# Optimization experiments

Measured on AMD Instinct MI355X. Metric: run time of the kernel, lower is better.

The kernel has to match this reference:

```python
import jax, jax.numpy as jnp
import numpy as np

NUM_CLASSES = 20
NUM_ANCHORS = 5
INPUT_SIZE = 320.0
CONF_THR = 0.5
IOU_THR = 0.5
EPS = 1e-6
H = W = 40


def setup_inputs() -> dict:
    key = jax.random.key(0)
    x = jax.random.normal(key, (1, NUM_ANCHORS * (5 + NUM_CLASSES), H, W), dtype=jnp.float32)
    scaled_anchors = jnp.array(
        [[1.3221, 1.73145], [3.19275, 4.00944], [5.05587, 8.09892],
         [9.47112, 4.84053], [11.2364, 10.0071]], dtype=jnp.float32)
    return {"x": x, "scaled_anchors": scaled_anchors}


def decode(x, anchors):
    # x: (B, A*(5+C), H, W) -> boxes (B, A*H*W, 6) = [cx, cy, w, h, conf, cls]
    B, _, h, w = x.shape
    A = anchors.shape[0]
    stride_h = INPUT_SIZE / h
    stride_w = INPUT_SIZE / w
    pred = x.reshape(B, A, 5 + NUM_CLASSES, h, w).transpose(0, 1, 3, 4, 2)  # (B,A,H,W,5+C)
    tx = jax.nn.sigmoid(pred[..., 0])
    ty = jax.nn.sigmoid(pred[..., 1])
    tw = pred[..., 2]
    th = pred[..., 3]
    conf = jax.nn.sigmoid(pred[..., 4])
    cls_idx = jnp.argmax(jax.nn.sigmoid(pred[..., 5:]), axis=-1)  # (B,A,H,W)
    grid_x = jnp.arange(w, dtype=x.dtype)            # broadcasts along last axis
    grid_y = jnp.arange(h, dtype=x.dtype)[:, None]   # broadcasts along row axis
    aw = anchors[:, 0][None, :, None, None]
    ah = anchors[:, 1][None, :, None, None]
    bx = (tx + grid_x) * stride_w
    by = (ty + grid_y) * stride_h
    bw = jnp.exp(tw) * aw * stride_w
    bh = jnp.exp(th) * ah * stride_h
    boxes = jnp.stack([bx, by, bw, bh, conf], axis=-1).reshape(B, -1, 5)
    cls_f = cls_idx.reshape(B, -1, 1).astype(x.dtype)
    return jnp.concatenate([boxes, cls_f], axis=-1)


def nms(boxes6):
    # boxes6: (N, 6) [cx, cy, w, h, conf, cls]. Fixed-shape NMS: boxes are
    # sorted by conf desc; suppressed / low-conf boxes are zeroed out.
    order = jnp.argsort(-boxes6[:, 4])
    b = boxes6[order]
    valid = b[:, 4] > CONF_THR
    cx, cy, w, h, cls = b[:, 0], b[:, 1], b[:, 2], b[:, 3], b[:, 5]
    x1, y1 = cx - w / 2.0, cy - h / 2.0
    x2, y2 = cx + w / 2.0, cy + h / 2.0
    inter_w = jnp.clip(jnp.minimum(x2[:, None], x2[None, :]) - jnp.maximum(x1[:, None], x1[None, :]), 0)
    inter_h = jnp.clip(jnp.minimum(y2[:, None], y2[None, :]) - jnp.maximum(y1[:, None], y1[None, :]), 0)
    inter = inter_w * inter_h                       # (N, N)
    area = jnp.abs((x2 - x1) * (y2 - y1))
    iou = inter / (area[:, None] + area[None, :] - inter + EPS)
    N = b.shape[0]
    idx = jnp.arange(N)

    def body(i, keep):
        # kept box i suppresses later boxes of the same class with IoU >= thr
        sup = keep[i] & keep & (cls == cls[i]) & (iou[i] >= IOU_THR) & (idx > i)
        return keep & ~sup

    keep = jax.lax.fori_loop(0, N, body, valid)
    return b * keep[:, None].astype(b.dtype)


def reference(x, scaled_anchors):
    dec = decode(x, scaled_anchors)   # (1, N, 6)
    return nms(dec[0])                # (N, 6)
```

## Files before the change

### kernel.cpp

```cpp
#include <hip/hip_runtime.h>
#include <stdint.h>

#define NBOX 8000
#define NPAD 8192

#define ECNT_OFF 0
#define SB(i)    (0x10000 + (size_t)(i) * 0x8000)
#define EDGE_OFF (size_t)0x200000

__device__ __forceinline__ float sigmoidf_(float x) {
    return 1.0f / (1.0f + expf(-x));
}

__global__ __launch_bounds__(512) void sort_decode_kernel(const float* __restrict__ x,
                                                          const float* __restrict__ anchors,
                                                          unsigned char* __restrict__ ws) {
    __shared__ unsigned long long keys[NPAD];
    __shared__ int partial[512];
    int tid  = threadIdx.x;
    int lane = tid & 63;
    int wv   = tid >> 6;
    int b    = blockIdx.x;

    if (b == 0 && tid == 0) *(unsigned int*)(ws + ECNT_OFF) = 0u;

    for (int t = tid; t < NPAD; t += 512) {
        unsigned long long k;
        if (t < NBOX) {
            int a = t / 1600, pos = t - a * 1600;
            float c = sigmoidf_(x[a * 40000 + 4 * 1600 + pos]);
            k = ((unsigned long long)__float_as_uint(c) << 32) | (unsigned long long)(8191 - t);
        } else {
            k = (unsigned long long)(8191 - t);
        }
        keys[t] = k;
    }
    __syncthreads();

    int i = (b << 6) + lane;
    unsigned long long ki = keys[i];
    const unsigned long long* ks = &keys[wv << 10];
    int cnt = 0;
    #pragma unroll 8
    for (int jj = 0; jj < 1024; ++jj) cnt += (ks[jj] > ki) ? 1 : 0;
    partial[(wv << 6) + lane] = cnt;
    __syncthreads();

    if (wv == 0) {
        int r = 0;
        #pragma unroll
        for (int s = 0; s < 8; ++s) r += partial[(s << 6) + lane];

        float bx = 0.f, by = 0.f, bw = 0.f, bh = 0.f, conf = 0.f, cls = -1.0f;
        if (i < NBOX) {
            int a = i / 1600, pos = i - a * 1600;
            int gy = pos / 40, gx = pos - gy * 40;
            const float* p = x + (size_t)a * 40000 + pos;
            float tx = sigmoidf_(p[0]);
            float ty = sigmoidf_(p[1600]);
            float tw = p[2 * 1600];
            float th = p[3 * 1600];
            conf = sigmoidf_(p[4 * 1600]);
            float best = -1.0f; int bi = 0;
            #pragma unroll
            for (int c = 0; c < 20; ++c) {
                float v = sigmoidf_(p[(5 + c) * 1600]);
                if (v > best) { best = v; bi = c; }
            }
            float aw = anchors[a * 2 + 0];
            float ah = anchors[a * 2 + 1];
            bx = (tx + (float)gx) * 8.0f;
            by = (ty + (float)gy) * 8.0f;
            bw = expf(tw) * aw * 8.0f;
            bh = expf(th) * ah * 8.0f;
            cls = (float)bi;
        }
        {
        #pragma clang fp contract(off)
            float x1 = bx - bw / 2.0f, y1 = by - bh / 2.0f;
            float x2 = bx + bw / 2.0f, y2 = by + bh / 2.0f;
            float ar = fabsf((x2 - x1) * (y2 - y1));
            ((float*)(ws + SB(0)))[r]  = bx;  ((float*)(ws + SB(1)))[r]  = by;
            ((float*)(ws + SB(2)))[r]  = bw;  ((float*)(ws + SB(3)))[r]  = bh;
            ((float*)(ws + SB(4)))[r]  = conf; ((float*)(ws + SB(5)))[r] = cls;
            ((float*)(ws + SB(6)))[r]  = x1;  ((float*)(ws + SB(7)))[r]  = y1;
            ((float*)(ws + SB(8)))[r]  = x2;  ((float*)(ws + SB(9)))[r]  = y2;
            ((float*)(ws + SB(10)))[r] = ar;
        }
    }
}

__global__ __launch_bounds__(256) void mask_kernel(unsigned char* __restrict__ ws) {
#pragma clang fp contract(off)
    const float* sconf = (const float*)(ws + SB(4));
    int i0 = blockIdx.y * 256;
    int w  = blockIdx.x;
    int j0 = w * 64;
    if (sconf[i0] <= 0.5f) return;
    if (sconf[j0] <= 0.5f) return;
    if (j0 + 64 <= i0) return;
    int tid  = threadIdx.x;
    int lane = tid & 63;
    int i    = i0 + tid;

    const float* sx1 = (const float*)(ws + SB(6));
    const float* sy1 = (const float*)(ws + SB(7));
    const float* sx2 = (const float*)(ws + SB(8));
    const float* sy2 = (const float*)(ws + SB(9));
    const float* sar = (const float*)(ws + SB(10));
    const float* scl = (const float*)(ws + SB(5));

    __shared__ float cx1[64], cy1[64], cx2[64], cy2[64], car[64], ccl[64], ccf[64];
    if (tid < 64) {
        int j = j0 + tid;
        cx1[tid] = sx1[j]; cy1[tid] = sy1[j];
        cx2[tid] = sx2[j]; cy2[tid] = sy2[j];
        car[tid] = sar[j]; ccl[tid] = scl[j]; ccf[tid] = sconf[j];
    }
    __syncthreads();

    unsigned long long word = 0;
    if (sconf[i] > 0.5f && j0 + 64 > i + 1) {
        float x1i = sx1[i], y1i = sy1[i], x2i = sx2[i], y2i = sy2[i];
        float ai = sar[i], ci = scl[i];
        for (int jj = 0; jj < 64; ++jj) {
            int j = j0 + jj;
            if (j <= i) continue;
            if (ccf[jj] <= 0.5f) continue;
            if (ccl[jj] != ci) continue;
            float iw = fminf(x2i, cx2[jj]) - fmaxf(x1i, cx1[jj]);
            iw = fmaxf(iw, 0.0f);
            float ih = fminf(y2i, cy2[jj]) - fmaxf(y1i, cy1[jj]);
            ih = fmaxf(ih, 0.0f);
            float inter = iw * ih;
            float denom = ai + car[jj] - inter + 1e-6f;
            if (inter / denom >= 0.5f) word |= (1ull << jj);
        }
    }

    int pc = __popcll(word);
    int scan = pc;
    #pragma unroll
    for (int d = 1; d < 64; d <<= 1) {
        int t = __shfl_up(scan, d, 64);
        if (lane >= d) scan += t;
    }
    int total = __shfl(scan, 63, 64);
    if (total > 0) {
        unsigned int base = 0;
        if (lane == 63)
            base = atomicAdd((unsigned int*)(ws + ECNT_OFF), (unsigned int)total);
        base = (unsigned int)__shfl((int)base, 63, 64);
        unsigned int off = base + (unsigned int)(scan - pc);
        unsigned int* edges = (unsigned int*)(ws + EDGE_OFF);
        unsigned long long t = word;
        while (t) {
            int bit = __builtin_ctzll(t);
            t &= t - 1ull;
            edges[off++] = ((unsigned int)i << 13) | (unsigned int)(j0 + bit);
        }
    }
}

__global__ __launch_bounds__(1024, 1) void nms_out_kernel(unsigned char* __restrict__ ws,
                                                          float* __restrict__ out) {
    int tid  = threadIdx.x;
    int lane = tid & 63;
    unsigned int E = *(const unsigned int*)(ws + ECNT_OFF);
    const unsigned int* edges = (const unsigned int*)(ws + EDGE_OFF);
    const float* sconf = (const float*)(ws + SB(4));

    __shared__ unsigned long long valid[128], alive[128], supp[128];
    __shared__ int flag;

    for (int c = tid >> 6; c < 128; c += 16) {
        unsigned long long m = __ballot(sconf[(c << 6) + lane] > 0.5f);
        if (lane == 0) valid[c] = m;
    }
    __syncthreads();
    if (tid < 128) alive[tid] = valid[tid];
    __syncthreads();

    for (;;) {
        if (tid < 128) supp[tid] = 0ull;
        __syncthreads();
        for (unsigned int e = tid; e < E; e += 1024) {
            unsigned int u = edges[e];
            unsigned int i = u >> 13, j = u & 8191u;
            if ((alive[i >> 6] >> (i & 63)) & 1ull)
                atomicOr(&supp[j >> 6], 1ull << (j & 63));
        }
        if (tid == 0) flag = 0;
        __syncthreads();
        if (tid < 128) {
            unsigned long long na = valid[tid] & ~supp[tid];
            if (na != alive[tid]) { alive[tid] = na; flag = 1; }
        }
        __syncthreads();
        if (!flag) break;
    }

    for (int r = tid; r < NBOX; r += 1024) {
        bool keep = (alive[r >> 6] >> (r & 63)) & 1ull;
        float o0 = 0.f, o1 = 0.f, o2 = 0.f, o3 = 0.f, o4 = 0.f, o5 = 0.f;
        if (keep) {
            o0 = ((const float*)(ws + SB(0)))[r];
            o1 = ((const float*)(ws + SB(1)))[r];
            o2 = ((const float*)(ws + SB(2)))[r];
            o3 = ((const float*)(ws + SB(3)))[r];
            o4 = ((const float*)(ws + SB(4)))[r];
            o5 = ((const float*)(ws + SB(5)))[r];
        }
        out[r * 6 + 0] = o0;
        out[r * 6 + 1] = o1;
        out[r * 6 + 2] = o2;
        out[r * 6 + 3] = o3;
        out[r * 6 + 4] = o4;
        out[r * 6 + 5] = o5;
    }
}

extern "C" void kernel_launch(void* const* d_in, const int* in_sizes, int n_in,
                              void* d_out, int out_size, void* d_ws, size_t ws_size,
                              hipStream_t stream) {
    const float* x       = (const float*)d_in[0];
    const float* anchors = (const float*)d_in[1];
    float* out           = (float*)d_out;
    unsigned char* ws    = (unsigned char*)d_ws;

    sort_decode_kernel<<<NPAD / 64, 512, 0, stream>>>(x, anchors, ws);
    dim3 mgrid(128, NPAD / 256);
    mask_kernel<<<mgrid, 256, 0, stream>>>(ws);
    nms_out_kernel<<<1, 1024, 0, stream>>>(ws, out);
}
```

Measured before the change: 120.2 us.

## Fuse mask and NMS kernels via last-block-done pattern with shared edge cache

Merges the IoU edge-building kernel and the single-block iterative NMS/output kernel into one launch. The last block to finish, found through an atomic done counter, runs the suppression fixed-point loop. It first copies the edge list into LDS when the edge count fits, so each iteration reads edges from LDS instead of global memory. Mask blocks grow to 1024 threads covering 1024 rows each, which cuts the block count but gives coarser early-exit skipping and a heavier per-block LDS footprint.

```diff
diff --git a/kernel.cpp b/kernel.cpp
--- a/kernel.cpp
+++ b/kernel.cpp
@@ -3,8 +3,10 @@
 
 #define NBOX 8000
 #define NPAD 8192
+#define ECAP 16384
 
 #define ECNT_OFF 0
+#define DONE_OFF 4
 #define SB(i)    (0x10000 + (size_t)(i) * 0x8000)
 #define EDGE_OFF (size_t)0x200000
 
@@ -22,7 +24,8 @@
     int wv   = tid >> 6;
     int b    = blockIdx.x;
 
-    if (b == 0 && tid == 0) *(unsigned int*)(ws + ECNT_OFF) = 0u;
+    if (b == 0 && tid == 0)
+        *(unsigned long long*)(ws + ECNT_OFF) = 0ull;
 
     for (int t = tid; t < NPAD; t += 512) {
         unsigned long long k;
@@ -90,93 +93,103 @@
     }
 }
 
-__global__ __launch_bounds__(256) void mask_kernel(unsigned char* __restrict__ ws) {
+__global__ __launch_bounds__(1024) void mask_nms_kernel(unsigned char* __restrict__ ws,
+                                                        float* __restrict__ out) {
 #pragma clang fp contract(off)
+    __shared__ float cx1[64], cy1[64], cx2[64], cy2[64], car[64], ccl[64], ccf[64];
+    __shared__ unsigned int eshare[ECAP];
+    __shared__ unsigned long long valid[128], alive[128], supp[128];
+    __shared__ int flag, isLast;
+
     const float* sconf = (const float*)(ws + SB(4));
-    int i0 = blockIdx.y * 256;
-    int w  = blockIdx.x;
-    int j0 = w * 64;
-    if (sconf[i0] <= 0.5f) return;
-    if (sconf[j0] <= 0.5f) return;
-    if (j0 + 64 <= i0) return;
     int tid  = threadIdx.x;
     int lane = tid & 63;
-    int i    = i0 + tid;
-
-    const float* sx1 = (const float*)(ws + SB(6));
-    const float* sy1 = (const float*)(ws + SB(7));
-    const float* sx2 = (const float*)(ws + SB(8));
-    const float* sy2 = (const float*)(ws + SB(9));
-    const float* sar = (const float*)(ws + SB(10));
-    const float* scl = (const float*)(ws + SB(5));
-
-    __shared__ float cx1[64], cy1[64], cx2[64], cy2[64], car[64], ccl[64], ccf[64];
-    if (tid < 64) {
-        int j = j0 + tid;
-        cx1[tid] = sx1[j]; cy1[tid] = sy1[j];
-        cx2[tid] = sx2[j]; cy2[tid] = sy2[j];
-        car[tid] = sar[j]; ccl[tid] = scl[j]; ccf[tid] = sconf[j];
-    }
-    __syncthreads();
-
-    unsigned long long word = 0;
-    if (sconf[i] > 0.5f && j0 + 64 > i + 1) {
-        float x1i = sx1[i], y1i = sy1[i], x2i = sx2[i], y2i = sy2[i];
-        float ai = sar[i], ci = scl[i];
-        for (int jj = 0; jj < 64; ++jj) {
-            int j = j0 + jj;
-            if (j <= i) continue;
-            if (ccf[jj] <= 0.5f) continue;
-            if (ccl[jj] != ci) continue;
-            float iw = fminf(x2i, cx2[jj]) - fmaxf(x1i, cx1[jj]);
-            iw = fmaxf(iw, 0.0f);
-            float ih = fminf(y2i, cy2[jj]) - fmaxf(y1i, cy1[jj]);
-            ih = fmaxf(ih, 0.0f);
-            float inter = iw * ih;
-            float denom = ai + car[jj] - inter + 1e-6f;
-            if (inter / denom >= 0.5f) word |= (1ull << jj);
-        }
-    }
-
-    int pc = __popcll(word);
-    int scan = pc;
-    #pragma unroll
-    for (int d = 1; d < 64; d <<= 1) {
-        int t = __shfl_up(scan, d, 64);
-        if (lane >= d) scan += t;
-    }
-    int total = __shfl(scan, 63, 64);
-    if (total > 0) {
-        unsigned int base = 0;
-        if (lane == 63)
-            base = atomicAdd((unsigned int*)(ws + ECNT_OFF), (unsigned int)total);
-        base = (unsigned int)__shfl((int)base, 63, 64);
-        unsigned int off = base + (unsigned int)(scan - pc);
-        unsigned int* edges = (unsigned int*)(ws + EDGE_OFF);
-        unsigned long long t = word;
-        while (t) {
-            int bit = __builtin_ctzll(t);
-            t &= t - 1ull;
-            edges[off++] = ((unsigned int)i << 13) | (unsigned int)(j0 + bit);
-        }
-    }
-}
-
-__global__ __launch_bounds__(1024, 1) void nms_out_kernel(unsigned char* __restrict__ ws,
-                                                          float* __restrict__ out) {
-    int tid  = threadIdx.x;
-    int lane = tid & 63;
-    unsigned int E = *(const unsigned int*)(ws + ECNT_OFF);
+    int w  = blockIdx.x;
+    int it = blockIdx.y;
+    int i0 = it << 10;
+    int j0 = w << 6;
+
+    bool skip = (sconf[i0] <= 0.5f) | (sconf[j0] <= 0.5f) | (j0 + 64 <= i0);
+    if (!skip) {
+        const float* sx1 = (const float*)(ws + SB(6));
+        const float* sy1 = (const float*)(ws + SB(7));
+        const float* sx2 = (const float*)(ws + SB(8));
+        const float* sy2 = (const float*)(ws + SB(9));
+        const float* sar = (const float*)(ws + SB(10));
+        const float* scl = (const float*)(ws + SB(5));
+        if (tid < 64) {
+            int j = j0 + tid;
+            cx1[tid] = sx1[j]; cy1[tid] = sy1[j];
+            cx2[tid] = sx2[j]; cy2[tid] = sy2[j];
+            car[tid] = sar[j]; ccl[tid] = scl[j]; ccf[tid] = sconf[j];
+        }
+        __syncthreads();
+
+        int i = i0 + tid;
+        unsigned long long word = 0;
+        if (sconf[i] > 0.5f && j0 + 64 > i + 1) {
+            float x1i = sx1[i], y1i = sy1[i], x2i = sx2[i], y2i = sy2[i];
+            float ai = sar[i], ci = scl[i];
+            for (int jj = 0; jj < 64; ++jj) {
+                int j = j0 + jj;
+                if (j <= i) continue;
+                if (ccf[jj] <= 0.5f) continue;
+                if (ccl[jj] != ci) continue;
+                float iw = fminf(x2i, cx2[jj]) - fmaxf(x1i, cx1[jj]);
+                iw = fmaxf(iw, 0.0f);
+                float ih = fminf(y2i, cy2[jj]) - fmaxf(y1i, cy1[jj]);
+                ih = fmaxf(ih, 0.0f);
+                float inter = iw * ih;
+                float denom = ai + car[jj] - inter + 1e-6f;
+                if (inter / denom >= 0.5f) word |= (1ull << jj);
+            }
+        }
+
+        int pc = __popcll(word);
+        int scan = pc;
+        #pragma unroll
+        for (int d = 1; d < 64; d <<= 1) {
+            int t = __shfl_up(scan, d, 64);
+            if (lane >= d) scan += t;
+        }
+        int total = __shfl(scan, 63, 64);
+        if (total > 0) {
+            unsigned int base = 0;
+            if (lane == 63)
+                base = atomicAdd((unsigned int*)(ws + ECNT_OFF), (unsigned int)total);
+            base = (unsigned int)__shfl((int)base, 63, 64);
+            unsigned int off = base + (unsigned int)(scan - pc);
+            unsigned int* edges = (unsigned int*)(ws + EDGE_OFF);
+            unsigned long long t = word;
+            int i_ = i0 + tid;
+            while (t) {
+                int bit = __builtin_ctzll(t);
+                t &= t - 1ull;
+                edges[off++] = ((unsigned int)i_ << 13) | (unsigned int)(j0 + bit);
+            }
+        }
+    }
+
+    __syncthreads();
+    if (tid == 0) {
+        __threadfence();
+        unsigned int old = __hip_atomic_fetch_add((unsigned int*)(ws + DONE_OFF), 1u,
+                                                  __ATOMIC_ACQ_REL, __HIP_MEMORY_SCOPE_AGENT);
+        isLast = (old == (int)(128 * 8 - 1));
+    }
+    __syncthreads();
+    if (!isLast) return;
+    __threadfence();
+
+    unsigned int E = *(volatile unsigned int*)(ws + ECNT_OFF);
     const unsigned int* edges = (const unsigned int*)(ws + EDGE_OFF);
-    const float* sconf = (const float*)(ws + SB(4));
-
-    __shared__ unsigned long long valid[128], alive[128], supp[128];
-    __shared__ int flag;
 
     for (int c = tid >> 6; c < 128; c += 16) {
         unsigned long long m = __ballot(sconf[(c << 6) + lane] > 0.5f);
         if (lane == 0) valid[c] = m;
     }
+    bool inl = (E <= (unsigned int)ECAP);
+    if (inl) for (unsigned int e = tid; e < E; e += 1024) eshare[e] = edges[e];
     __syncthreads();
     if (tid < 128) alive[tid] = valid[tid];
     __syncthreads();
@@ -185,7 +198,7 @@
         if (tid < 128) supp[tid] = 0ull;
         __syncthreads();
         for (unsigned int e = tid; e < E; e += 1024) {
-            unsigned int u = edges[e];
+            unsigned int u = inl ? eshare[e] : edges[e];
             unsigned int i = u >> 13, j = u & 8191u;
             if ((alive[i >> 6] >> (i & 63)) & 1ull)
                 atomicOr(&supp[j >> 6], 1ull << (j & 63));
@@ -229,7 +242,6 @@
     unsigned char* ws    = (unsigned char*)d_ws;
 
     sort_decode_kernel<<<NPAD / 64, 512, 0, stream>>>(x, anchors, ws);
-    dim3 mgrid(128, NPAD / 256);
-    mask_kernel<<<mgrid, 256, 0, stream>>>(ws);
-    nms_out_kernel<<<1, 1024, 0, stream>>>(ws, out);
-}
+    dim3 mgrid(128, 8);
+    mask_nms_kernel<<<mgrid, 1024, 0, stream>>>(ws, out);
+}
```

New measurement: 129.8 us. +8.0%, slower.

## Resolve NMS suppression segment-by-segment with register-cached edges

Applied to the files above, without the earlier changes.

Replaces the global fixed-point iteration over all suppression edges with a segmented sweep. The 8192 sorted boxes are split into 16 segments of 512, each segment is iterated to convergence using only its internal edges, and then its surviving boxes push suppression forward to later segments. Edges are cached in per-thread registers when there are at most 16384 of them, so repeated passes avoid global reloads. This is meant to cut the number of full-edge-list passes, but every segment now scans all cached edges and pays barrier overhead, and register use rises. The old global loop is kept as a fallback for larger edge counts.

```diff
diff --git a/kernel.cpp b/kernel.cpp
--- a/kernel.cpp
+++ b/kernel.cpp
@@ -3,6 +3,9 @@
 
 #define NBOX 8000
 #define NPAD 8192
+#define ECAP 16384
+#define SEGW 8
+#define NSEG 16
 
 #define ECNT_OFF 0
 #define SB(i)    (0x10000 + (size_t)(i) * 0x8000)
@@ -167,37 +170,86 @@
     int tid  = threadIdx.x;
     int lane = tid & 63;
     unsigned int E = *(const unsigned int*)(ws + ECNT_OFF);
-    const unsigned int* edges = (const unsigned int*)(ws + EDGE_OFF);
+    const unsigned int* gedges = (const unsigned int*)(ws + EDGE_OFF);
     const float* sconf = (const float*)(ws + SB(4));
 
-    __shared__ unsigned long long valid[128], alive[128], supp[128];
+    __shared__ unsigned long long valid[128], alive[128], suppExt[128], suppInt[SEGW];
     __shared__ int flag;
 
     for (int c = tid >> 6; c < 128; c += 16) {
         unsigned long long m = __ballot(sconf[(c << 6) + lane] > 0.5f);
         if (lane == 0) valid[c] = m;
     }
+    if (tid < 128) suppExt[tid] = 0ull;
     __syncthreads();
     if (tid < 128) alive[tid] = valid[tid];
     __syncthreads();
 
-    for (;;) {
-        if (tid < 128) supp[tid] = 0ull;
-        __syncthreads();
-        for (unsigned int e = tid; e < E; e += 1024) {
-            unsigned int u = edges[e];
-            unsigned int i = u >> 13, j = u & 8191u;
-            if ((alive[i >> 6] >> (i & 63)) & 1ull)
-                atomicOr(&supp[j >> 6], 1ull << (j & 63));
-        }
-        if (tid == 0) flag = 0;
-        __syncthreads();
-        if (tid < 128) {
-            unsigned long long na = valid[tid] & ~supp[tid];
-            if (na != alive[tid]) { alive[tid] = na; flag = 1; }
-        }
-        __syncthreads();
-        if (!flag) break;
+    if (E <= (unsigned int)ECAP) {
+        unsigned int eu[ECAP / 1024];
+        int ne = 0;
+        for (unsigned int e = tid; e < E; e += 1024) eu[ne++] = gedges[e];
+
+        for (int s = 0; s < NSEG; ++s) {
+            bool segv = false;
+            #pragma unroll
+            for (int k = 0; k < SEGW; ++k) segv |= (valid[s * SEGW + k] != 0ull);
+            if (!segv) continue;
+
+            for (;;) {
+                if (tid < SEGW) suppInt[tid] = 0ull;
+                if (tid == 0) flag = 0;
+                __syncthreads();
+                for (int k = 0; k < ne; ++k) {
+                    unsigned int u = eu[k];
+                    unsigned int i = u >> 13, j = u & 8191u;
+                    if ((int)(i >> 9) == s && (int)(j >> 9) == s &&
+                        ((alive[i >> 6] >> (i & 63)) & 1ull))
+                        atomicOr(&suppInt[(j >> 6) - s * SEGW], 1ull << (j & 63));
+                }
+                __syncthreads();
+                if (tid < SEGW) {
+                    int w = s * SEGW + tid;
+                    unsigned long long na = valid[w] & ~suppExt[w] & ~suppInt[tid];
+                    if (na != alive[w]) { alive[w] = na; flag = 1; }
+                }
+                __syncthreads();
+                if (!flag) break;
+            }
+            for (int k = 0; k < ne; ++k) {
+                unsigned int u = eu[k];
+                unsigned int i = u >> 13, j = u & 8191u;
+                if ((int)(i >> 9) == s && (int)(j >> 9) > s &&
+                    ((alive[i >> 6] >> (i & 63)) & 1ull))
+                    atomicOr(&suppExt[j >> 6], 1ull << (j & 63));
+            }
+            __syncthreads();
+            if (tid < 128) {
+                int w = tid;
+                if ((w >> 3) > s) alive[w] = valid[w] & ~suppExt[w];
+            }
+            __syncthreads();
+        }
+    } else {
+        __shared__ unsigned long long supp[128];
+        for (;;) {
+            if (tid < 128) supp[tid] = 0ull;
+            if (tid == 0) flag = 0;
+            __syncthreads();
+            for (unsigned int e = tid; e < E; e += 1024) {
+                unsigned int u = gedges[e];
+                unsigned int i = u >> 13, j = u & 8191u;
+                if ((alive[i >> 6] >> (i & 63)) & 1ull)
+                    atomicOr(&supp[j >> 6], 1ull << (j & 63));
+            }
+            __syncthreads();
+            if (tid < 128) {
+                unsigned long long na = valid[tid] & ~supp[tid];
+                if (na != alive[tid]) { alive[tid] = na; flag = 1; }
+            }
+            __syncthreads();
+            if (!flag) break;
+        }
     }
 
     for (int r = tid; r < NBOX; r += 1024) {
```

Measured after the change: 128.7 us. +7.1%, slower.
